# Optimization experiments

Hardware: AMD Instinct MI355X
Metric: run time of the kernel (lower is better)

The kernel has to match this reference:

```python
import jax, jax.numpy as jnp
import numpy as np

NULL_IDX = 0  # word_to_idx['<NULL>']
N, T, D, WV, H, V = 128, 65, 512, 128, 128, 10000


def setup_inputs() -> dict:
    key = jax.random.key(0)
    ks = jax.random.split(key, 12)
    scale = 0.02
    return {
        "features": jax.random.normal(ks[0], (N, D), dtype=jnp.float32),
        "captions": jax.random.randint(ks[1], (N, T), 0, V, dtype=jnp.int32),
        # TemporalAffine(input_dim, hidden_dim)
        "W_proj": jax.random.normal(ks[2], (D, H), dtype=jnp.float32) * scale,
        "b_proj": jnp.zeros((H,), dtype=jnp.float32),
        # nn.Embedding(vocab_size, wordvec_dim)
        "embed": jax.random.normal(ks[3], (V, WV), dtype=jnp.float32) * scale,
        # nn.RNN(wordvec_dim, hidden_dim, num_layers=1) weights
        "W_ih": jax.random.normal(ks[4], (H, WV), dtype=jnp.float32) * scale,
        "W_hh": jax.random.normal(ks[5], (H, H), dtype=jnp.float32) * scale,
        "b_ih": jnp.zeros((H,), dtype=jnp.float32),
        "b_hh": jnp.zeros((H,), dtype=jnp.float32),
        # TemporalAffine(hidden_dim, vocab_size)
        "W_vocab": jax.random.normal(ks[6], (H, V), dtype=jnp.float32) * scale,
        "b_vocab": jnp.zeros((V,), dtype=jnp.float32),
    }


def reference(features, captions, W_proj, b_proj, embed, W_ih, W_hh, b_ih, b_hh, W_vocab, b_vocab):
    captions_in = captions[:, :-1]   # (N, T-1)
    captions_out = captions[:, 1:]   # (N, T-1)
    mask = (captions_out != NULL_IDX).astype(jnp.float32)

    # initial hidden state: affine projection of image features (no tanh)
    h0 = features @ W_proj + b_proj                      # (N, H)

    # word embeddings, time-major for scan
    x = embed[captions_in]                               # (N, T-1, WV)
    x_tm = jnp.swapaxes(x, 0, 1)                          # (T-1, N, WV)

    def step(h_prev, x_t):
        # vanilla RNN cell: tanh(x W_ih^T + b_ih + h W_hh^T + b_hh)
        h_new = jnp.tanh(x_t @ W_ih.T + b_ih + h_prev @ W_hh.T + b_hh)
        return h_new, h_new

    _, hs = jax.lax.scan(step, h0, x_tm)                  # (T-1, N, H)
    h = jnp.swapaxes(hs, 0, 1)                            # (N, T-1, H)

    # temporal affine to vocab scores
    scores = h @ W_vocab + b_vocab                        # (N, T-1, V)

    # temporal softmax loss, masked, averaged over batch size N
    logp = jax.nn.log_softmax(scores, axis=-1)
    nll = -jnp.take_along_axis(logp, captions_out[..., None], axis=-1)[..., 0]
    loss = jnp.sum(nll * mask) / captions.shape[0]
    return loss
```

## Files before the change

kernel.cpp:

```cpp
#include <hip/hip_runtime.h>
#include <hip/hip_bf16.h>
#include <math.h>

typedef __attribute__((ext_vector_type(8))) short short8;
typedef __attribute__((ext_vector_type(4))) float f32x4;
typedef __attribute__((ext_vector_type(4))) unsigned int u32x4;

#define NB   128
#define TT   64
#define DD   512
#define HH   128
#define WVD  128
#define VV   10000
#define VP   10048
#define NROW (NB*TT)
#define NTILE (VP/64)
#define VT   32
#define TILE_BYTES 16384
#define LOG2E 1.44269504088896f
#define LN2   0.69314718055995f

__device__ __forceinline__ unsigned short f2bf(float x) {
  union { float f; unsigned int u; } v; v.f = x;
  unsigned int r = v.u + 0x7fffu + ((v.u >> 16) & 1u);
  return (unsigned short)(r >> 16);
}
__device__ __forceinline__ float bf2f(unsigned short u) {
  union { unsigned int i; float f; } v; v.i = ((unsigned int)u) << 16; return v.f;
}

__global__ __launch_bounds__(256) void k_prep(
    const float* __restrict__ Wv, unsigned short* __restrict__ Wvt,
    const float* __restrict__ Wih, float* __restrict__ Wt,
    const float* __restrict__ bv, float* __restrict__ expbv,
    float* __restrict__ out,
    const float* __restrict__ features, const float* __restrict__ Wp,
    const float* __restrict__ bp, float* __restrict__ h0) {
  __shared__ float tile[64][65];
  int b = blockIdx.x, tid = threadIdx.x;
  if (b < 314) {
    int bvv = (b >> 1) * 64;
    int bk  = (b & 1) * 64;
    int tv = tid & 63;
    int tk0 = tid >> 6;
    #pragma unroll
    for (int kk = 0; kk < 64; kk += 4) {
      int k = bk + kk + tk0;
      int v = bvv + tv;
      tile[kk + tk0][tv] = (v < VV) ? Wv[(size_t)k*VV + v] : 0.f;
    }
    __syncthreads();
    int tk = tid & 63;
    int tv0 = tid >> 6;
    #pragma unroll
    for (int vv = 0; vv < 64; vv += 4) {
      int v = bvv + vv + tv0;
      Wvt[(size_t)v*HH + bk + tk] = f2bf(tile[tk][vv + tv0]);
    }
  } else if (b < 378) {
    int o = (b - 314)*256 + tid;
    int k = o >> 7, j = o & 127;
    Wt[o] = Wih[j*WVD + k];
  } else if (b < 418) {
    int v = (b - 378)*256 + tid;
    if (v < VP) expbv[v] = (v < VV) ? __expf(bv[v]) : 0.f;
  } else if (b == 418) {
    if (tid == 0) out[0] = 0.f;
  } else {
    int n = b - 419;
    float* fl  = &tile[0][0];
    f32x4* red = (f32x4*)&tile[20][0];
    fl[tid]       = features[n*DD + tid];
    fl[tid + 256] = features[n*DD + 256 + tid];
    __syncthreads();
    int jq = (tid & 31) * 4;
    int ks = tid >> 5;
    f32x4 acc = {0.f,0.f,0.f,0.f};
    const float* wp = Wp + (size_t)(ks*64)*HH + jq;
    #pragma unroll 4
    for (int k = 0; k < 64; ++k) {
      f32x4 wv = *(const f32x4*)(wp + (size_t)k*HH);
      acc += fl[ks*64 + k] * wv;
    }
    red[ks*32 + (tid & 31)] = acc;
    __syncthreads();
    if (tid < 32) {
      f32x4 s = red[tid];
      #pragma unroll
      for (int i = 1; i < 8; ++i) s += red[i*32 + tid];
      s += *(const f32x4*)(bp + tid*4);
      *(f32x4*)(h0 + n*HH + tid*4) = s;
    }
  }
}

__global__ __launch_bounds__(256) void k_xb(const int* __restrict__ captions,
    const float* __restrict__ embed, const float* __restrict__ Wt,
    const float* __restrict__ bih, const float* __restrict__ bhh,
    float* __restrict__ xb) {
  int g = blockIdx.x*256 + threadIdx.x;
  int jq = (g & 31) * 4;
  int r  = g >> 5;
  int n = r >> 6, t = r & 63;
  const float* x = embed + (size_t)captions[n*65 + t] * WVD;
  f32x4 acc = *(const f32x4*)(bih + jq);
  acc += *(const f32x4*)(bhh + jq);
  #pragma unroll 4
  for (int k = 0; k < WVD; k += 4) {
    f32x4 xv = *(const f32x4*)(x + k);
    const float* wp = Wt + (size_t)k*HH + jq;
    f32x4 w0 = *(const f32x4*)(wp);
    f32x4 w1 = *(const f32x4*)(wp + HH);
    f32x4 w2 = *(const f32x4*)(wp + 2*HH);
    f32x4 w3 = *(const f32x4*)(wp + 3*HH);
    acc += xv[0]*w0;
    acc += xv[1]*w1;
    acc += xv[2]*w2;
    acc += xv[3]*w3;
  }
  *(f32x4*)(xb + (size_t)r*HH + jq) = acc;
}

__global__ __launch_bounds__(256) void k_rnn(const float* __restrict__ h0,
    const float* __restrict__ xb, const float* __restrict__ Whh,
    unsigned short* __restrict__ hsb) {
  __shared__ float xl[TT][HH];
  __shared__ unsigned short hl[TT][HH];
  __shared__ float hbuf[2][HH];
  int n = blockIdx.x, tid = threadIdx.x;
  int w = tid >> 6, l = tid & 63;
  int j = w*32 + (l & 31);
  int kb = (l >> 5) * 64;

  const float* xsrc = xb + (size_t)n*TT*HH;
  #pragma unroll
  for (int it = 0; it < 8; ++it) {
    int o = it*256 + tid;
    *(f32x4*)(&xl[0][0] + o*4) = *(const f32x4*)(xsrc + o*4);
  }
  float wr_[64];
  const float* wsrc = Whh + (size_t)j*HH + kb;
  #pragma unroll
  for (int i = 0; i < 16; ++i) {
    f32x4 v = *(const f32x4*)(wsrc + i*4);
    wr_[i*4+0]=v[0]; wr_[i*4+1]=v[1]; wr_[i*4+2]=v[2]; wr_[i*4+3]=v[3];
  }
  if (tid < HH) hbuf[0][tid] = h0[n*HH + tid];
  __syncthreads();

  int cur = 0;
  for (int t = 0; t < TT; ++t) {
    float s0=0.f, s1=0.f, s2=0.f, s3=0.f;
    const float* hr = &hbuf[cur][kb];
    #pragma unroll
    for (int i = 0; i < 16; ++i) {
      f32x4 hv = *(const f32x4*)(hr + i*4);
      s0 += hv[0]*wr_[i*4+0]; s1 += hv[1]*wr_[i*4+1];
      s2 += hv[2]*wr_[i*4+2]; s3 += hv[3]*wr_[i*4+3];
    }
    float s = (s0+s1)+(s2+s3);
    s += __shfl_xor(s, 32);
    float v = s + xl[t][j];
    float e = __builtin_amdgcn_exp2f(v * (2.0f*LOG2E));
    float h = 1.0f - 2.0f*__builtin_amdgcn_rcpf(e + 1.0f);
    if (l < 32) {
      hbuf[cur^1][j] = h;
      hl[t][j] = f2bf(h * LOG2E);
    }
    __syncthreads();
    cur ^= 1;
  }
  unsigned short* dst = hsb + (size_t)n*TT*HH;
  #pragma unroll
  for (int it = 0; it < 4; ++it) {
    int o = it*256 + tid;
    *(u32x4*)(dst + o*8) = *(const u32x4*)(&hl[0][0] + o*8);
  }
}

__global__ __launch_bounds__(256) void k_loss(
    const unsigned short* __restrict__ hsb,
    const unsigned short* __restrict__ wvt,
    const float* __restrict__ expbv,
    float* __restrict__ se_part) {
  __shared__ unsigned short bt[2][TILE_BYTES/2];
  int tid = threadIdx.x;
  int w = tid >> 6, l = tid & 63;
  int l4 = l >> 4, lc = l & 15;
  int rb = blockIdx.x >> 5;
  int vt = blockIdx.x & 31;
  int wrow = rb*256 + w*64;

  short8 af[4][4];
  #pragma unroll
  for (int sm = 0; sm < 4; ++sm)
    #pragma unroll
    for (int ks = 0; ks < 4; ++ks)
      af[sm][ks] = *(const short8*)(hsb + (size_t)(wrow + sm*16 + lc)*HH + ks*32 + l4*8);

  int T = (lc & 7) << 4;
  int sb[4];
  #pragma unroll
  for (int ks = 0; ks < 4; ++ks) sb[ks] = ((ks*64) + l4*16) ^ T;

#define STAGE(bufi, ct) do {                                                  \
    const char* _gb = (const char*)wvt + (size_t)(ct)*TILE_BYTES;             \
    _Pragma("unroll")                                                         \
    for (int q = 0; q < 4; ++q) {                                             \
      int _off = w*4096 + q*1024 + l*16;                                      \
      int _src = _off ^ (((_off >> 8) & 7) << 4);                             \
      __builtin_amdgcn_global_load_lds(                                       \
        (const __attribute__((address_space(1))) void*)(_gb + _src),          \
        (__attribute__((address_space(3))) void*)((char*)&bt[bufi][0] + w*4096 + q*1024), \
        16, 0, 0);                                                            \
    }                                                                         \
  } while (0)

#define EBLOAD(dst, ct) do {                                                  \
    const float* _e = expbv + (ct)*64 + lc;                                   \
    dst[0] = _e[0]; dst[1] = _e[16]; dst[2] = _e[32]; dst[3] = _e[48];        \
  } while (0)

#define COMPUTE(bufi, ebv_) do {                                              \
    const char* _Bb = (const char*)&bt[bufi][0];                              \
    _Pragma("unroll")                                                         \
    for (int st = 0; st < 4; ++st) {                                          \
      const char* _Bs = _Bb + st*4096 + lc*256;                               \
      short8 _b0 = *(const short8*)(_Bs + sb[0]);                             \
      short8 _b1 = *(const short8*)(_Bs + sb[1]);                             \
      short8 _b2 = *(const short8*)(_Bs + sb[2]);                             \
      short8 _b3 = *(const short8*)(_Bs + sb[3]);                             \
      float _eb = ebv_[st];                                                   \
      _Pragma("unroll")                                                       \
      for (int sm = 0; sm < 4; ++sm) {                                        \
        f32x4 _acc = {0.f,0.f,0.f,0.f};                                       \
        _acc = __builtin_amdgcn_mfma_f32_16x16x32_bf16(af[sm][0], _b0, _acc, 0,0,0); \
        _acc = __builtin_amdgcn_mfma_f32_16x16x32_bf16(af[sm][1], _b1, _acc, 0,0,0); \
        _acc = __builtin_amdgcn_mfma_f32_16x16x32_bf16(af[sm][2], _b2, _acc, 0,0,0); \
        _acc = __builtin_amdgcn_mfma_f32_16x16x32_bf16(af[sm][3], _b3, _acc, 0,0,0); \
        _Pragma("unroll")                                                     \
        for (int jj = 0; jj < 4; ++jj)                                        \
          se[sm][jj] = fmaf(__builtin_amdgcn_exp2f(_acc[jj]), _eb, se[sm][jj]); \
      }                                                                       \
    }                                                                         \
  } while (0)

  float se[4][4] = {{0.f}};
  float ebc[4], ebn[4];
  STAGE(0, vt);
  EBLOAD(ebc, vt);
  __syncthreads();
  int i = 0;
  for (;;) {
    int nextct = vt + (i+1)*VT;
    if (nextct < NTILE) { STAGE((i+1)&1, nextct); EBLOAD(ebn, nextct); }
    COMPUTE(i&1, ebc);
    if (nextct >= NTILE) break;
    __syncthreads();
    ebc[0]=ebn[0]; ebc[1]=ebn[1]; ebc[2]=ebn[2]; ebc[3]=ebn[3];
    ++i;
  }

  #pragma unroll
  for (int sm = 0; sm < 4; ++sm)
    #pragma unroll
    for (int jj = 0; jj < 4; ++jj) {
      float v = se[sm][jj];
      v += __shfl_xor(v, 1); v += __shfl_xor(v, 2);
      v += __shfl_xor(v, 4); v += __shfl_xor(v, 8);
      se[sm][jj] = v;
    }
  if (lc == 0) {
    #pragma unroll
    for (int sm = 0; sm < 4; ++sm)
      #pragma unroll
      for (int jj = 0; jj < 4; ++jj)
        se_part[(size_t)vt*NROW + wrow + sm*16 + l4*4 + jj] = se[sm][jj];
  }
#undef STAGE
#undef EBLOAD
#undef COMPUTE
}

__global__ __launch_bounds__(256) void k_final(
    const unsigned short* __restrict__ hsb,
    const unsigned short* __restrict__ wvt,
    const float* __restrict__ bv,
    const float* __restrict__ se_part,
    const int* __restrict__ captions,
    float* __restrict__ out) {
  int tid = threadIdx.x;
  int w = tid >> 6, l = tid & 63;
  int row = blockIdx.x*32 + w*8 + (l >> 3);
  int seg = l & 7;
  int n = row >> 6, t = row & 63;
  int tg = captions[n*65 + t + 1];
  float sep = 0.f;
  #pragma unroll
  for (int i = 0; i < 4; ++i)
    sep += se_part[(size_t)(seg*4 + i)*NROW + row];
  float part = 0.f;
  if (tg != 0) {
    const unsigned short* a = hsb + (size_t)row*HH + seg*16;
    const unsigned short* b = wvt + (size_t)tg*HH + seg*16;
    short8 a0 = *(const short8*)a, a1 = *(const short8*)(a+8);
    short8 b0 = *(const short8*)b, b1 = *(const short8*)(b+8);
    #pragma unroll
    for (int i = 0; i < 8; ++i) {
      part += bf2f((unsigned short)a0[i]) * bf2f((unsigned short)b0[i]);
      part += bf2f((unsigned short)a1[i]) * bf2f((unsigned short)b1[i]);
    }
  }
  part += __shfl_xor(part, 1); sep += __shfl_xor(sep, 1);
  part += __shfl_xor(part, 2); sep += __shfl_xor(sep, 2);
  part += __shfl_xor(part, 4); sep += __shfl_xor(sep, 4);
  if (seg == 0 && tg != 0) {
    float score = part * LN2 + bv[tg];
    float nll = logf(sep) - score;
    atomicAdd(out, nll * (1.0f/128.0f));
  }
}

extern "C" void kernel_launch(void* const* d_in, const int* in_sizes, int n_in,
                              void* d_out, int out_size, void* d_ws, size_t ws_size,
                              hipStream_t stream) {
  const float* features = (const float*)d_in[0];
  const int*   captions = (const int*)d_in[1];
  const float* W_proj   = (const float*)d_in[2];
  const float* b_proj   = (const float*)d_in[3];
  const float* embed    = (const float*)d_in[4];
  const float* W_ih     = (const float*)d_in[5];
  const float* W_hh     = (const float*)d_in[6];
  const float* b_ih     = (const float*)d_in[7];
  const float* b_hh     = (const float*)d_in[8];
  const float* W_vocab  = (const float*)d_in[9];
  const float* b_vocab  = (const float*)d_in[10];
  float* out = (float*)d_out;
  char* ws = (char*)d_ws;

  float*          h0      = (float*)(ws + 0x000000);
  float*          xb      = (float*)(ws + 0x010000);
  float*          se_part = (float*)(ws + 0x010000);
  unsigned short* hsb     = (unsigned short*)(ws + 0x410000);
  float*          wih_t   = (float*)(ws + 0x610000);
  unsigned short* wvt     = (unsigned short*)(ws + 0x620000);
  float*          expbv   = (float*)(ws + 0x8A0000);

  hipLaunchKernelGGL(k_prep, dim3(547), dim3(256), 0, stream,
                     W_vocab, wvt, W_ih, wih_t, b_vocab, expbv, out,
                     features, W_proj, b_proj, h0);
  hipLaunchKernelGGL(k_xb,   dim3(NROW*32/256), dim3(256), 0, stream,
                     captions, embed, wih_t, b_ih, b_hh, xb);
  hipLaunchKernelGGL(k_rnn,  dim3(NB), dim3(256), 0, stream, h0, xb, W_hh, hsb);
  hipLaunchKernelGGL(k_loss, dim3(32*VT), dim3(256), 0, stream, hsb, wvt, expbv, se_part);
  hipLaunchKernelGGL(k_final, dim3(NROW/32), dim3(256), 0, stream,
                     hsb, wvt, b_vocab, se_part, captions, out);
}
```

Baseline: 111.4 us.

## Fuse prep, input projection and RNN into one kernel with MFMA x-projection

```diff
diff --git a/kernel.cpp b/kernel.cpp
--- a/kernel.cpp
+++ b/kernel.cpp
@@ -28,48 +28,71 @@
 __device__ __forceinline__ float bf2f(unsigned short u) {
   union { unsigned int i; float f; } v; v.i = ((unsigned int)u) << 16; return v.f;
 }
-
-__global__ __launch_bounds__(256) void k_prep(
+__device__ __forceinline__ short8 cvt2bf8(f32x4 a, f32x4 b) {
+  short8 t;
+  t[0]=(short)f2bf(a[0]); t[1]=(short)f2bf(a[1]);
+  t[2]=(short)f2bf(a[2]); t[3]=(short)f2bf(a[3]);
+  t[4]=(short)f2bf(b[0]); t[5]=(short)f2bf(b[1]);
+  t[6]=(short)f2bf(b[2]); t[7]=(short)f2bf(b[3]);
+  return t;
+}
+
+__global__ __launch_bounds__(256) void k_main(
     const float* __restrict__ Wv, unsigned short* __restrict__ Wvt,
-    const float* __restrict__ Wih, float* __restrict__ Wt,
     const float* __restrict__ bv, float* __restrict__ expbv,
     float* __restrict__ out,
     const float* __restrict__ features, const float* __restrict__ Wp,
-    const float* __restrict__ bp, float* __restrict__ h0) {
-  __shared__ float tile[64][65];
+    const float* __restrict__ bp,
+    const int* __restrict__ captions, const float* __restrict__ embed,
+    const float* __restrict__ Wih, const float* __restrict__ bih,
+    const float* __restrict__ bhh, const float* __restrict__ Whh,
+    unsigned short* __restrict__ hsb) {
+  __shared__ __align__(16) char smem[99328];
   int b = blockIdx.x, tid = threadIdx.x;
-  if (b < 314) {
-    int bvv = (b >> 1) * 64;
-    int bk  = (b & 1) * 64;
-    int tv = tid & 63;
-    int tk0 = tid >> 6;
-    #pragma unroll
-    for (int kk = 0; kk < 64; kk += 4) {
-      int k = bk + kk + tk0;
-      int v = bvv + tv;
-      tile[kk + tk0][tv] = (v < VV) ? Wv[(size_t)k*VV + v] : 0.f;
-    }
-    __syncthreads();
-    int tk = tid & 63;
-    int tv0 = tid >> 6;
-    #pragma unroll
-    for (int vv = 0; vv < 64; vv += 4) {
-      int v = bvv + vv + tv0;
-      Wvt[(size_t)v*HH + bk + tk] = f2bf(tile[tk][vv + tv0]);
-    }
-  } else if (b < 378) {
-    int o = (b - 314)*256 + tid;
-    int k = o >> 7, j = o & 127;
-    Wt[o] = Wih[j*WVD + k];
-  } else if (b < 418) {
-    int v = (b - 378)*256 + tid;
-    if (v < VP) expbv[v] = (v < VV) ? __expf(bv[v]) : 0.f;
-  } else if (b == 418) {
-    if (tid == 0) out[0] = 0.f;
-  } else {
-    int n = b - 419;
-    float* fl  = &tile[0][0];
-    f32x4* red = (f32x4*)&tile[20][0];
+
+  if (b >= 128) {
+    if (b < 442) {
+      float (*tile)[65] = (float (*)[65])smem;
+      int tb = b - 128;
+      int bvv = (tb >> 1) * 64;
+      int bk  = (tb & 1) * 64;
+      int tv = tid & 63;
+      int tk0 = tid >> 6;
+      #pragma unroll
+      for (int kk = 0; kk < 64; kk += 4) {
+        int k = bk + kk + tk0;
+        int v = bvv + tv;
+        tile[kk + tk0][tv] = (v < VV) ? Wv[(size_t)k*VV + v] : 0.f;
+      }
+      __syncthreads();
+      int tk = tid & 63;
+      int tv0 = tid >> 6;
+      #pragma unroll
+      for (int vv = 0; vv < 64; vv += 4) {
+        int v = bvv + vv + tv0;
+        Wvt[(size_t)v*HH + bk + tk] = f2bf(tile[tk][vv + tv0]);
+      }
+    } else if (b < 482) {
+      int v = (b - 442)*256 + tid;
+      if (v < VP) expbv[v] = (v < VV) ? __expf(bv[v]) : 0.f;
+    } else {
+      if (tid == 0) out[0] = 0.f;
+    }
+    return;
+  }
+
+  int n = b;
+  float* xl            = (float*)smem;
+  unsigned short* hl   = (unsigned short*)(smem + 32768);
+  char* xbf            = smem + 49152;
+  char* wihbf          = smem + 65536;
+  float* hbuf          = (float*)(smem + 98304);
+  int w = tid >> 6, l = tid & 63;
+  int l4 = l >> 4, lc = l & 15;
+
+  {
+    float* fl  = (float*)(smem + 32768);
+    f32x4* red = (f32x4*)(smem + 32768 + 2048);
     fl[tid]       = features[n*DD + tid];
     fl[tid + 256] = features[n*DD + 256 + tid];
     __syncthreads();
@@ -89,55 +112,33 @@
       #pragma unroll
       for (int i = 1; i < 8; ++i) s += red[i*32 + tid];
       s += *(const f32x4*)(bp + tid*4);
-      *(f32x4*)(h0 + n*HH + tid*4) = s;
-    }
-  }
-}
-
-__global__ __launch_bounds__(256) void k_xb(const int* __restrict__ captions,
-    const float* __restrict__ embed, const float* __restrict__ Wt,
-    const float* __restrict__ bih, const float* __restrict__ bhh,
-    float* __restrict__ xb) {
-  int g = blockIdx.x*256 + threadIdx.x;
-  int jq = (g & 31) * 4;
-  int r  = g >> 5;
-  int n = r >> 6, t = r & 63;
-  const float* x = embed + (size_t)captions[n*65 + t] * WVD;
-  f32x4 acc = *(const f32x4*)(bih + jq);
-  acc += *(const f32x4*)(bhh + jq);
-  #pragma unroll 4
-  for (int k = 0; k < WVD; k += 4) {
-    f32x4 xv = *(const f32x4*)(x + k);
-    const float* wp = Wt + (size_t)k*HH + jq;
-    f32x4 w0 = *(const f32x4*)(wp);
-    f32x4 w1 = *(const f32x4*)(wp + HH);
-    f32x4 w2 = *(const f32x4*)(wp + 2*HH);
-    f32x4 w3 = *(const f32x4*)(wp + 3*HH);
-    acc += xv[0]*w0;
-    acc += xv[1]*w1;
-    acc += xv[2]*w2;
-    acc += xv[3]*w3;
-  }
-  *(f32x4*)(xb + (size_t)r*HH + jq) = acc;
-}
-
-__global__ __launch_bounds__(256) void k_rnn(const float* __restrict__ h0,
-    const float* __restrict__ xb, const float* __restrict__ Whh,
-    unsigned short* __restrict__ hsb) {
-  __shared__ float xl[TT][HH];
-  __shared__ unsigned short hl[TT][HH];
-  __shared__ float hbuf[2][HH];
-  int n = blockIdx.x, tid = threadIdx.x;
-  int w = tid >> 6, l = tid & 63;
+      *(f32x4*)(hbuf + tid*4) = s;
+    }
+  }
+
+  {
+    int row = tid >> 1, half = tid & 1;
+    const float* src = Wih + (size_t)row*WVD + half*64;
+    #pragma unroll
+    for (int i = 0; i < 8; ++i) {
+      f32x4 a = *(const f32x4*)(src + i*8);
+      f32x4 c = *(const f32x4*)(src + i*8 + 4);
+      int chunk = half*8 + i;
+      *(short8*)(wihbf + row*256 + ((chunk << 4) ^ ((row & 7) << 4))) = cvt2bf8(a, c);
+    }
+    int rt = tid >> 2, seg = tid & 3;
+    int token = captions[n*65 + rt];
+    const float* xs = embed + (size_t)token*WVD + seg*32;
+    #pragma unroll
+    for (int i = 0; i < 4; ++i) {
+      f32x4 a = *(const f32x4*)(xs + i*8);
+      f32x4 c = *(const f32x4*)(xs + i*8 + 4);
+      int chunk = seg*4 + i;
+      *(short8*)(xbf + rt*256 + ((chunk << 4) ^ ((rt & 7) << 4))) = cvt2bf8(a, c);
+    }
+  }
   int j = w*32 + (l & 31);
   int kb = (l >> 5) * 64;
-
-  const float* xsrc = xb + (size_t)n*TT*HH;
-  #pragma unroll
-  for (int it = 0; it < 8; ++it) {
-    int o = it*256 + tid;
-    *(f32x4*)(&xl[0][0] + o*4) = *(const f32x4*)(xsrc + o*4);
-  }
   float wr_[64];
   const float* wsrc = Whh + (size_t)j*HH + kb;
   #pragma unroll
@@ -145,13 +146,36 @@
     f32x4 v = *(const f32x4*)(wsrc + i*4);
     wr_[i*4+0]=v[0]; wr_[i*4+1]=v[1]; wr_[i*4+2]=v[2]; wr_[i*4+3]=v[3];
   }
-  if (tid < HH) hbuf[0][tid] = h0[n*HH + tid];
+  __syncthreads();
+
+  {
+    short8 axf[4];
+    int rowa = w*16 + lc;
+    #pragma unroll
+    for (int ks = 0; ks < 4; ++ks)
+      axf[ks] = *(const short8*)(xbf + rowa*256 + (((ks*4 + l4) << 4) ^ ((rowa & 7) << 4)));
+    #pragma unroll
+    for (int ct = 0; ct < 8; ++ct) {
+      int rowb = ct*16 + lc;
+      f32x4 acc = {0.f,0.f,0.f,0.f};
+      #pragma unroll
+      for (int ks = 0; ks < 4; ++ks) {
+        short8 bf = *(const short8*)(wihbf + rowb*256 + (((ks*4 + l4) << 4) ^ ((rowb & 7) << 4)));
+        acc = __builtin_amdgcn_mfma_f32_16x16x32_bf16(axf[ks], bf, acc, 0, 0, 0);
+      }
+      int col = ct*16 + lc;
+      float bb = bih[col] + bhh[col];
+      #pragma unroll
+      for (int jj = 0; jj < 4; ++jj)
+        xl[(w*16 + l4*4 + jj)*HH + col] = acc[jj] + bb;
+    }
+  }
   __syncthreads();
 
   int cur = 0;
   for (int t = 0; t < TT; ++t) {
     float s0=0.f, s1=0.f, s2=0.f, s3=0.f;
-    const float* hr = &hbuf[cur][kb];
+    const float* hr = hbuf + cur*HH + kb;
     #pragma unroll
     for (int i = 0; i < 16; ++i) {
       f32x4 hv = *(const f32x4*)(hr + i*4);
@@ -160,12 +184,12 @@
     }
     float s = (s0+s1)+(s2+s3);
     s += __shfl_xor(s, 32);
-    float v = s + xl[t][j];
+    float v = s + xl[t*HH + j];
     float e = __builtin_amdgcn_exp2f(v * (2.0f*LOG2E));
     float h = 1.0f - 2.0f*__builtin_amdgcn_rcpf(e + 1.0f);
     if (l < 32) {
-      hbuf[cur^1][j] = h;
-      hl[t][j] = f2bf(h * LOG2E);
+      hbuf[(cur^1)*HH + j] = h;
+      hl[t*HH + j] = f2bf(h * LOG2E);
     }
     __syncthreads();
     cur ^= 1;
@@ -174,7 +198,7 @@
   #pragma unroll
   for (int it = 0; it < 4; ++it) {
     int o = it*256 + tid;
-    *(u32x4*)(dst + o*8) = *(const u32x4*)(&hl[0][0] + o*8);
+    *(u32x4*)(dst + o*8) = *(const u32x4*)(hl + o*8);
   }
 }
 
@@ -302,9 +326,9 @@
   float part = 0.f;
   if (tg != 0) {
     const unsigned short* a = hsb + (size_t)row*HH + seg*16;
-    const unsigned short* b = wvt + (size_t)tg*HH + seg*16;
+    const unsigned short* bq = wvt + (size_t)tg*HH + seg*16;
     short8 a0 = *(const short8*)a, a1 = *(const short8*)(a+8);
-    short8 b0 = *(const short8*)b, b1 = *(const short8*)(b+8);
+    short8 b0 = *(const short8*)bq, b1 = *(const short8*)(bq+8);
     #pragma unroll
     for (int i = 0; i < 8; ++i) {
       part += bf2f((unsigned short)a0[i]) * bf2f((unsigned short)b0[i]);
@@ -338,21 +362,17 @@
   float* out = (float*)d_out;
   char* ws = (char*)d_ws;
 
-  float*          h0      = (float*)(ws + 0x000000);
-  float*          xb      = (float*)(ws + 0x010000);
   float*          se_part = (float*)(ws + 0x010000);
   unsigned short* hsb     = (unsigned short*)(ws + 0x410000);
-  float*          wih_t   = (float*)(ws + 0x610000);
   unsigned short* wvt     = (unsigned short*)(ws + 0x620000);
   float*          expbv   = (float*)(ws + 0x8A0000);
 
-  hipLaunchKernelGGL(k_prep, dim3(547), dim3(256), 0, stream,
-                     W_vocab, wvt, W_ih, wih_t, b_vocab, expbv, out,
-                     features, W_proj, b_proj, h0);
-  hipLaunchKernelGGL(k_xb,   dim3(NROW*32/256), dim3(256), 0, stream,
-                     captions, embed, wih_t, b_ih, b_hh, xb);
-  hipLaunchKernelGGL(k_rnn,  dim3(NB), dim3(256), 0, stream, h0, xb, W_hh, hsb);
-  hipLaunchKernelGGL(k_loss, dim3(32*VT), dim3(256), 0, stream, hsb, wvt, expbv, se_part);
+  hipLaunchKernelGGL(k_main, dim3(483), dim3(256), 0, stream,
+                     W_vocab, wvt, b_vocab, expbv, out,
+                     features, W_proj, b_proj, captions, embed,
+                     W_ih, b_ih, b_hh, W_hh, hsb);
+  hipLaunchKernelGGL(k_loss, dim3(32*VT), dim3(256), 0, stream,
+                     hsb, wvt, expbv, se_part);
   hipLaunchKernelGGL(k_final, dim3(NROW/32), dim3(256), 0, stream,
                      hsb, wvt, b_vocab, se_part, captions, out);
 }
```

Result: faster. 94.17 us (-15.5%).
